# Performance work log

Hardware: AMD Instinct MI355X
Metric: run time of the kernel (lower is better)

Reference implementation:

```python
import jax, jax.numpy as jnp
import numpy as np

NUM_LEVELS = 8
BASE_RES = 32
MAX_RES = 2048
FEAT_DIM = 8
MAX_TABLE = 2 ** 19
WIDTH = 256
DEPTH = 8
NUM_FREQS = 4
N = 1048576

RESOLUTIONS = [min(BASE_RES * 2 ** l, MAX_RES) for l in range(NUM_LEVELS)]
TABLE_SIZES = [min(r ** 3, MAX_TABLE) for r in RESOLUTIONS]
POS_DIM = NUM_LEVELS * FEAT_DIM            # 64
VIEW_DIM = 3 + 3 * 2 * NUM_FREQS          # 27
IN_DIM = POS_DIM + VIEW_DIM                # 91


def _xavier(key, shape):
    fan_in, fan_out = shape[-2], shape[-1]
    limit = float(np.sqrt(6.0 / (fan_in + fan_out)))
    return jax.random.uniform(key, shape, jnp.float32, -limit, limit)


def setup_inputs() -> dict:
    key = jax.random.key(0)
    ks = jax.random.split(key, 32)
    inp = {
        'positions': jax.random.uniform(ks[0], (N, 3), jnp.float32),  # in [0,1) subset of [-1,1]
        'viewdirs': jax.random.normal(ks[1], (N, 3), jnp.float32),
    }
    for l in range(NUM_LEVELS):
        inp[f'table{l}'] = _xavier(ks[2 + l], (TABLE_SIZES[l], FEAT_DIM))
    inp['w0'] = _xavier(ks[12], (IN_DIM, WIDTH))
    inp['b0'] = jnp.zeros((WIDTH,), jnp.float32)
    # 6 hidden (with ReLU) + 1 final (no ReLU) 256x256 linears, stacked
    inp['wh'] = _xavier(ks[13], (DEPTH - 1, WIDTH, WIDTH))
    inp['bh'] = jnp.zeros((DEPTH - 1, WIDTH), jnp.float32)
    inp['wd'] = _xavier(ks[14], (WIDTH, 1))
    inp['bd'] = jnp.zeros((1,), jnp.float32)
    inp['wc'] = _xavier(ks[15], (WIDTH, 3))
    inp['bc'] = jnp.zeros((3,), jnp.float32)
    return inp


def _hash_encode(positions, table, res):
    # (p + 1) * 0.5 * res, clamped to [0, res-1]
    ps = jnp.clip((positions + 1.0) * (0.5 * res), 0.0, res - 1.0)
    idx_f = ps[..., 0] * (res * res) + ps[..., 1] * res + ps[..., 2]
    # clamp in float first so int32 cast is safe (matches torch clamp-to-table)
    idx = jnp.clip(idx_f, 0.0, table.shape[0] - 1.0).astype(jnp.int32)
    return table[idx]  # [..., FEAT_DIM]


def _view_encode(v):
    feats = [v]
    for f in range(NUM_FREQS):
        feats.append(jnp.sin((2.0 ** f) * jnp.pi * v))
        feats.append(jnp.cos((2.0 ** f) * jnp.pi * v))
    return jnp.concatenate(feats, axis=-1)


def reference(positions, viewdirs, table0, table1, table2, table3, table4,
              table5, table6, table7, w0, b0, wh, bh, wd, bd, wc, bc):
    tables = [table0, table1, table2, table3, table4, table5, table6, table7]
    spatial = jnp.concatenate(
        [_hash_encode(positions, tables[l], RESOLUTIONS[l]) for l in range(NUM_LEVELS)],
        axis=-1)                                           # [N, 64]
    feats = jnp.concatenate([spatial, _view_encode(viewdirs)], axis=-1)  # [N, 91]

    x = jax.nn.relu(feats @ w0 + b0)
    for i in range(DEPTH - 2):                             # 6 hidden layers with ReLU
        x = jax.nn.relu(x @ wh[i] + bh[i])
    x = x @ wh[DEPTH - 2] + bh[DEPTH - 2]                  # final linear, no ReLU

    density = x @ wd + bd                                  # [N, 1]
    color = jax.nn.sigmoid(x @ wc + bc)                    # [N, 3]
    return density, color
```

## Files before the change

kernel.cpp:

```cpp
#include <hip/hip_runtime.h>
#include <math.h>

#define N_PTS 1048576

typedef _Float16 half8 __attribute__((ext_vector_type(8)));
typedef _Float16 half4v __attribute__((ext_vector_type(4)));
typedef float float4v __attribute__((ext_vector_type(4)));
typedef float f32x16 __attribute__((ext_vector_type(16)));

#define W0T_OFF 0
#define WHT_OFF 24576
#define WHEAD_OFF 483328
#define WS_HALVES 487424

__global__ void prep_weights(const float* __restrict__ w0,
                             const float* __restrict__ wh,
                             const float* __restrict__ wd,
                             const float* __restrict__ wc,
                             _Float16* __restrict__ ws) {
  int stride = gridDim.x * blockDim.x;
  for (int i = blockIdx.x * blockDim.x + threadIdx.x; i < WS_HALVES; i += stride) {
    float v;
    if (i < WHT_OFF) {
      int kb = i >> 11, n = (i >> 3) & 255, j = i & 7;
      int k = kb * 8 + j;
      v = (k < 91) ? w0[k * 256 + n] : 0.0f;
    } else if (i < WHEAD_OFF) {
      int rel = i - WHT_OFF;
      int layer = rel >> 16;
      int r = rel & 65535;
      int kb = r >> 11, n = (r >> 3) & 255, j = r & 7;
      int k = kb * 8 + j;
      v = wh[(layer << 16) + k * 256 + n];
    } else {
      int rel = i - WHEAD_OFF;
      int n = rel >> 8, k = rel & 255;
      v = (n == 0) ? wd[k] : ((n < 4) ? wc[k * 3 + n - 1] : 0.0f);
    }
    ws[i] = (_Float16)v;
  }
}

__device__ __forceinline__ int xaddr(int m, int kb) {
  return m * 512 + (kb ^ ((m & 15) << 4));
}

template <int KB>
__device__ __forceinline__ void mlp_layer(char* X, const _Float16* __restrict__ Wt,
                                          size_t laneoff,
                                          const float* __restrict__ bias, bool relu,
                                          int wn, int lr5, int lg2) {
  f32x16 acc[2][4];
#pragma unroll
  for (int nt = 0; nt < 2; ++nt)
#pragma unroll
    for (int q = 0; q < 4; ++q) {
      float4v bv = *(const float4v*)(bias + wn * 64 + nt * 32 + q * 8 + lg2 * 4);
#pragma unroll
      for (int mt = 0; mt < 4; ++mt)
#pragma unroll
        for (int rr = 0; rr < 4; ++rr) acc[nt][mt][q * 4 + rr] = bv[rr];
    }

  const _Float16* wb = Wt + laneoff;
  const int swz = (lr5 & 15) << 4;
  const int cbase = lg2 * 16;
  const int row0 = lr5 * 512;

  half8 a0 = *(const half8*)wb;
  half8 a1 = *(const half8*)(wb + 256);
#pragma unroll
  for (int ks = 0; ks < KB; ++ks) {
    half8 a0n = a0, a1n = a1;
    if (ks + 1 < KB) {
      a0n = *(const half8*)(wb + (size_t)(ks + 1) * 4096);
      a1n = *(const half8*)(wb + (size_t)(ks + 1) * 4096 + 256);
    }
    const int c = (ks * 32 + cbase) ^ swz;
    half8 b[4];
#pragma unroll
    for (int mt = 0; mt < 4; ++mt)
      b[mt] = *(const half8*)&X[row0 + mt * 32 * 512 + c];
#pragma unroll
    for (int mt = 0; mt < 4; ++mt) {
      acc[0][mt] = __builtin_amdgcn_mfma_f32_32x32x16_f16(a0, b[mt], acc[0][mt], 0, 0, 0);
      acc[1][mt] = __builtin_amdgcn_mfma_f32_32x32x16_f16(a1, b[mt], acc[1][mt], 0, 0, 0);
    }
    a0 = a0n;
    a1 = a1n;
  }
  __syncthreads();

#pragma unroll
  for (int mt = 0; mt < 4; ++mt) {
    const int rowb = (mt * 32 + lr5) * 512;
#pragma unroll
    for (int nt = 0; nt < 2; ++nt)
#pragma unroll
      for (int q = 0; q < 4; ++q) {
        half4v hv;
#pragma unroll
        for (int rr = 0; rr < 4; ++rr) {
          float y = acc[nt][mt][q * 4 + rr];
          if (relu) y = fmaxf(y, 0.0f);
          hv[rr] = (_Float16)y;
        }
        *(half4v*)&X[rowb + ((wn * 128 + nt * 64 + q * 16 + lg2 * 8) ^ swz)] = hv;
      }
  }
  __syncthreads();
}

__global__ __launch_bounds__(256, 2) void nerf_fused(
    const float* __restrict__ pos, const float* __restrict__ vdir,
    const float* __restrict__ t0, const float* __restrict__ t1,
    const float* __restrict__ t2, const float* __restrict__ t3,
    const float* __restrict__ t4, const float* __restrict__ t5,
    const float* __restrict__ t6, const float* __restrict__ t7,
    const float* __restrict__ b0, const float* __restrict__ bh,
    const float* __restrict__ bd, const float* __restrict__ bc,
    const _Float16* __restrict__ ws, float* __restrict__ out) {
  __shared__ __align__(16) char X[65536];
  const int tid = threadIdx.x;
  const int wg = blockIdx.x;
  const int m = tid & 127;
  const int p = wg * 128 + m;

  if (tid < 128) {
    const float px = pos[p * 3], py = pos[p * 3 + 1], pz = pos[p * 3 + 2];
    const float* tabs[8] = {t0, t1, t2, t3, t4, t5, t6, t7};
    const int resi[8] = {32, 64, 128, 256, 512, 1024, 2048, 2048};
    const float tmax[8] = {32767.0f, 262143.0f, 524287.0f, 524287.0f,
                           524287.0f, 524287.0f, 524287.0f, 524287.0f};
#pragma unroll
    for (int lv = 0; lv < 8; ++lv) {
      const float r = (float)resi[lv];
      const float hr = 0.5f * r;
      const float rm1 = r - 1.0f;
      float cx = fminf(fmaxf(__fmul_rn(__fadd_rn(px, 1.0f), hr), 0.0f), rm1);
      float cy = fminf(fmaxf(__fmul_rn(__fadd_rn(py, 1.0f), hr), 0.0f), rm1);
      float cz = fminf(fmaxf(__fmul_rn(__fadd_rn(pz, 1.0f), hr), 0.0f), rm1);
      float idxf = __fadd_rn(__fadd_rn(__fmul_rn(cx, r * r), __fmul_rn(cy, r)), cz);
      idxf = fminf(fmaxf(idxf, 0.0f), tmax[lv]);
      int idx = (int)idxf;
      const float4* row = (const float4*)(tabs[lv] + (size_t)idx * 8);
      float4 f0 = row[0], f1 = row[1];
      half8 h;
      h[0] = (_Float16)f0.x; h[1] = (_Float16)f0.y;
      h[2] = (_Float16)f0.z; h[3] = (_Float16)f0.w;
      h[4] = (_Float16)f1.x; h[5] = (_Float16)f1.y;
      h[6] = (_Float16)f1.z; h[7] = (_Float16)f1.w;
      *(half8*)&X[xaddr(m, lv * 16)] = h;
    }
  } else {
    float v0 = vdir[p * 3], v1 = vdir[p * 3 + 1], v2 = vdir[p * 3 + 2];
    const float cf[4] = {(float)(M_PI), (float)(2.0 * M_PI),
                         (float)(4.0 * M_PI), (float)(8.0 * M_PI)};
    float feat[32];
    feat[0] = v0; feat[1] = v1; feat[2] = v2;
    float vv[3] = {v0, v1, v2};
#pragma unroll
    for (int f = 0; f < 4; ++f)
#pragma unroll
      for (int d = 0; d < 3; ++d) {
        float arg = __fmul_rn(cf[f], vv[d]);
        feat[3 + f * 6 + d] = __sinf(arg);
        feat[6 + f * 6 + d] = __cosf(arg);
      }
#pragma unroll
    for (int i = 27; i < 32; ++i) feat[i] = 0.0f;
#pragma unroll
    for (int s = 0; s < 4; ++s) {
      half8 h;
#pragma unroll
      for (int j = 0; j < 8; ++j) h[j] = (_Float16)feat[s * 8 + j];
      *(half8*)&X[xaddr(m, 128 + s * 16)] = h;
    }
  }
  __syncthreads();

  const int lane = tid & 63;
  const int w = tid >> 6;
  const int lr5 = lane & 31;
  const int lg2 = lane >> 5;
  const size_t laneoff = ((size_t)(lg2 * 256 + w * 64 + lr5)) * 8;

  mlp_layer<6>(X, ws + W0T_OFF, laneoff, b0, true, w, lr5, lg2);
#pragma unroll 1
  for (int i = 0; i < 7; ++i)
    mlp_layer<16>(X, ws + WHT_OFF + (i << 16), laneoff, bh + (i << 8),
                  i < 6, w, lr5, lg2);

  const int lr = lane & 15;
  const int lg = lane >> 4;
  float4v hacc[2];
  {
    float bv = (lr == 0) ? bd[0] : ((lr < 4) ? bc[lr - 1] : 0.0f);
    hacc[0] = (float4v){bv, bv, bv, bv};
    hacc[1] = hacc[0];
  }
  const _Float16* Wh = ws + WHEAD_OFF;
#pragma unroll
  for (int ks = 0; ks < 8; ++ks) {
    half8 bfr = *(const half8*)(Wh + lr * 256 + ks * 32 + lg * 8);
#pragma unroll
    for (int mt = 0; mt < 2; ++mt) {
      half8 a = *(const half8*)&X[xaddr(w * 32 + mt * 16 + lr, ks * 64 + lg * 16)];
      hacc[mt] = __builtin_amdgcn_mfma_f32_16x16x32_f16(a, bfr, hacc[mt], 0, 0, 0);
    }
  }
#pragma unroll
  for (int mt = 0; mt < 2; ++mt)
#pragma unroll
    for (int r = 0; r < 4; ++r) {
      int pp = wg * 128 + w * 32 + mt * 16 + lg * 4 + r;
      float vv = hacc[mt][r];
      if (lr == 0) {
        out[pp] = vv;
      } else if (lr < 4) {
        out[N_PTS + 3 * pp + (lr - 1)] = 1.0f / (1.0f + __expf(-vv));
      }
    }
}

extern "C" void kernel_launch(void* const* d_in, const int* in_sizes, int n_in,
                              void* d_out, int out_size, void* d_ws, size_t ws_size,
                              hipStream_t stream) {
  const float* pos = (const float*)d_in[0];
  const float* vdir = (const float*)d_in[1];
  const float* t0 = (const float*)d_in[2];
  const float* t1 = (const float*)d_in[3];
  const float* t2 = (const float*)d_in[4];
  const float* t3 = (const float*)d_in[5];
  const float* t4 = (const float*)d_in[6];
  const float* t5 = (const float*)d_in[7];
  const float* t6 = (const float*)d_in[8];
  const float* t7 = (const float*)d_in[9];
  const float* w0 = (const float*)d_in[10];
  const float* b0 = (const float*)d_in[11];
  const float* wh = (const float*)d_in[12];
  const float* bh = (const float*)d_in[13];
  const float* wd = (const float*)d_in[14];
  const float* bd = (const float*)d_in[15];
  const float* wc = (const float*)d_in[16];
  const float* bc = (const float*)d_in[17];
  _Float16* ws = (_Float16*)d_ws;
  float* out = (float*)d_out;

  hipLaunchKernelGGL(prep_weights, dim3((WS_HALVES + 255) / 256), dim3(256), 0, stream,
                     w0, wh, wd, wc, ws);
  hipLaunchKernelGGL(nerf_fused, dim3(N_PTS / 128), dim3(256), 0, stream,
                     pos, vdir, t0, t1, t2, t3, t4, t5, t6, t7,
                     b0, bh, bd, bc, (const _Float16*)ws, out);
}
```

Before: 999.5 us.

## Re-tile activation LDS layout and prefetch LDS B fragments with MFMA priority

Replaces the row-major XOR-swizzled activation buffer in LDS with a tiled layout: 32-row blocks with k-chunk-major, 16-byte per-row slots. The aim is contiguous, conflict-free fragment reads for the MFMA operands. The inner GEMM loop now software-pipelines the LDS B-operand loads one k-step ahead, as it already did for the weights, and wraps the MFMA burst in s_setprio. The tiled layout may bring bank conflicts on the half4 epilogue stores and the head-layer reads, and the prefetch raises register pressure under the 2-blocks/SM launch bound.

After: 911.0 us. 1.1x faster.

```diff
diff --git a/kernel.cpp b/kernel.cpp
--- a/kernel.cpp
+++ b/kernel.cpp
@@ -41,8 +41,8 @@
   }
 }
 
-__device__ __forceinline__ int xaddr(int m, int kb) {
-  return m * 512 + (kb ^ ((m & 15) << 4));
+__device__ __forceinline__ int x2addr(int m, int kb) {
+  return (m >> 5) * 16384 + kb * 512 + (m & 31) * 16;
 }
 
 template <int KB>
@@ -63,37 +63,44 @@
     }
 
   const _Float16* wb = Wt + laneoff;
-  const int swz = (lr5 & 15) << 4;
-  const int cbase = lg2 * 16;
-  const int row0 = lr5 * 512;
+  const int broff = lg2 * 512 + lr5 * 16;
 
   half8 a0 = *(const half8*)wb;
   half8 a1 = *(const half8*)(wb + 256);
+  half8 bc0 = *(const half8*)&X[broff];
+  half8 bc1 = *(const half8*)&X[broff + 16384];
+  half8 bc2 = *(const half8*)&X[broff + 32768];
+  half8 bc3 = *(const half8*)&X[broff + 49152];
 #pragma unroll
   for (int ks = 0; ks < KB; ++ks) {
     half8 a0n = a0, a1n = a1;
+    half8 bn0 = bc0, bn1 = bc1, bn2 = bc2, bn3 = bc3;
     if (ks + 1 < KB) {
+      const int c = broff + (ks + 1) * 1024;
+      bn0 = *(const half8*)&X[c];
+      bn1 = *(const half8*)&X[c + 16384];
+      bn2 = *(const half8*)&X[c + 32768];
+      bn3 = *(const half8*)&X[c + 49152];
       a0n = *(const half8*)(wb + (size_t)(ks + 1) * 4096);
       a1n = *(const half8*)(wb + (size_t)(ks + 1) * 4096 + 256);
     }
-    const int c = (ks * 32 + cbase) ^ swz;
-    half8 b[4];
-#pragma unroll
-    for (int mt = 0; mt < 4; ++mt)
-      b[mt] = *(const half8*)&X[row0 + mt * 32 * 512 + c];
-#pragma unroll
-    for (int mt = 0; mt < 4; ++mt) {
-      acc[0][mt] = __builtin_amdgcn_mfma_f32_32x32x16_f16(a0, b[mt], acc[0][mt], 0, 0, 0);
-      acc[1][mt] = __builtin_amdgcn_mfma_f32_32x32x16_f16(a1, b[mt], acc[1][mt], 0, 0, 0);
-    }
-    a0 = a0n;
-    a1 = a1n;
+    __builtin_amdgcn_s_setprio(1);
+    acc[0][0] = __builtin_amdgcn_mfma_f32_32x32x16_f16(a0, bc0, acc[0][0], 0, 0, 0);
+    acc[1][0] = __builtin_amdgcn_mfma_f32_32x32x16_f16(a1, bc0, acc[1][0], 0, 0, 0);
+    acc[0][1] = __builtin_amdgcn_mfma_f32_32x32x16_f16(a0, bc1, acc[0][1], 0, 0, 0);
+    acc[1][1] = __builtin_amdgcn_mfma_f32_32x32x16_f16(a1, bc1, acc[1][1], 0, 0, 0);
+    acc[0][2] = __builtin_amdgcn_mfma_f32_32x32x16_f16(a0, bc2, acc[0][2], 0, 0, 0);
+    acc[1][2] = __builtin_amdgcn_mfma_f32_32x32x16_f16(a1, bc2, acc[1][2], 0, 0, 0);
+    acc[0][3] = __builtin_amdgcn_mfma_f32_32x32x16_f16(a0, bc3, acc[0][3], 0, 0, 0);
+    acc[1][3] = __builtin_amdgcn_mfma_f32_32x32x16_f16(a1, bc3, acc[1][3], 0, 0, 0);
+    __builtin_amdgcn_s_setprio(0);
+    a0 = a0n; a1 = a1n;
+    bc0 = bn0; bc1 = bn1; bc2 = bn2; bc3 = bn3;
   }
   __syncthreads();
 
 #pragma unroll
   for (int mt = 0; mt < 4; ++mt) {
-    const int rowb = (mt * 32 + lr5) * 512;
 #pragma unroll
     for (int nt = 0; nt < 2; ++nt)
 #pragma unroll
@@ -105,7 +112,7 @@
           if (relu) y = fmaxf(y, 0.0f);
           hv[rr] = (_Float16)y;
         }
-        *(half4v*)&X[rowb + ((wn * 128 + nt * 64 + q * 16 + lg2 * 8) ^ swz)] = hv;
+        *(half4v*)&X[mt * 16384 + (wn * 8 + nt * 4 + q) * 512 + lr5 * 16 + lg2 * 8] = hv;
       }
   }
   __syncthreads();
@@ -150,7 +157,7 @@
       h[2] = (_Float16)f0.z; h[3] = (_Float16)f0.w;
       h[4] = (_Float16)f1.x; h[5] = (_Float16)f1.y;
       h[6] = (_Float16)f1.z; h[7] = (_Float16)f1.w;
-      *(half8*)&X[xaddr(m, lv * 16)] = h;
+      *(half8*)&X[x2addr(m, lv)] = h;
     }
   } else {
     float v0 = vdir[p * 3], v1 = vdir[p * 3 + 1], v2 = vdir[p * 3 + 2];
@@ -174,7 +181,7 @@
       half8 h;
 #pragma unroll
       for (int j = 0; j < 8; ++j) h[j] = (_Float16)feat[s * 8 + j];
-      *(half8*)&X[xaddr(m, 128 + s * 16)] = h;
+      *(half8*)&X[x2addr(m, 8 + s)] = h;
     }
   }
   __syncthreads();
@@ -205,7 +212,7 @@
     half8 bfr = *(const half8*)(Wh + lr * 256 + ks * 32 + lg * 8);
 #pragma unroll
     for (int mt = 0; mt < 2; ++mt) {
-      half8 a = *(const half8*)&X[xaddr(w * 32 + mt * 16 + lr, ks * 64 + lg * 16)];
+      half8 a = *(const half8*)&X[x2addr(w * 32 + mt * 16 + lr, ks * 4 + lg)];
       hacc[mt] = __builtin_amdgcn_mfma_f32_16x16x32_f16(a, bfr, hacc[mt], 0, 0, 0);
     }
   }
```
